# Performance work log

Hardware: AMD Instinct MI355X
Metric: run time of the kernel (lower is better)

## Reference

```python
import jax, jax.numpy as jnp
import numpy as np

N_NODES = 100000
N_EDGES = 1600000
IN_DIM = 256
HIDDEN = 128
N_CLASSES = 40


def gcn_conv(x, W, b, src, dst, n_nodes):
    """torch_geometric GCNConv: transform -> add self-loops -> sym-normalized sum-aggregate -> +bias."""
    h = x @ W  # [N, out]
    loop = jnp.arange(n_nodes, dtype=src.dtype)
    src2 = jnp.concatenate([src, loop])
    dst2 = jnp.concatenate([dst, loop])
    # degree with self-loops (edge weight 1)
    deg = jax.ops.segment_sum(jnp.ones_like(dst2, dtype=h.dtype), dst2, num_segments=n_nodes)
    dinv = jnp.where(deg > 0, jax.lax.rsqrt(deg), 0.0)
    norm = dinv[src2] * dinv[dst2]  # [E+N]
    msg = h[src2] * norm[:, None]   # [E+N, out] gather + scale
    out = jax.ops.segment_sum(msg, dst2, num_segments=n_nodes)
    return out + b


def setup_inputs() -> dict:
    key = jax.random.key(0)
    k1, k2, k3, k4 = jax.random.split(key, 4)
    x = jax.random.normal(k1, (N_NODES, IN_DIM), dtype=jnp.float32)
    edge_index = jax.random.randint(k2, (2, N_EDGES), 0, N_NODES, dtype=jnp.int64)
    W1 = jax.random.normal(k3, (IN_DIM, HIDDEN), dtype=jnp.float32) * (1.0 / np.sqrt(IN_DIM))
    b1 = jnp.zeros((HIDDEN,), dtype=jnp.float32)
    W2 = jax.random.normal(k4, (HIDDEN, N_CLASSES), dtype=jnp.float32) * (1.0 / np.sqrt(HIDDEN))
    b2 = jnp.zeros((N_CLASSES,), dtype=jnp.float32)
    return {"x": x, "edge_index": edge_index, "W1": W1, "b1": b1, "W2": W2, "b2": b2}


def reference(x, edge_index, W1, b1, W2, b2):
    src, dst = edge_index[0], edge_index[1]
    h = gcn_conv(x, W1, b1, src, dst, N_NODES)
    h = jax.nn.relu(h)
    # dropout p=0.5 is identity in eval mode
    out = gcn_conv(h, W2, b2, src, dst, N_NODES)
    return out
```

## Files before the change

### kernel.cpp

```cpp
#include <hip/hip_runtime.h>
#include <hip/hip_bf16.h>
#include <hip/hip_fp16.h>

#define N_NODES 100000
#define N_EDGES 1600000
#define IN_DIM 256
#define HIDDEN 128
#define NCLS 40
#define NCLS_PAD 48

#define N_BUCKETS 256
#define NPB 391
#define BCAP 8192
#define EPT 16
#define BIN_WG 4096
#define BIN_BLOCKS 391

typedef __attribute__((ext_vector_type(8))) _Float16 half8;
typedef __attribute__((ext_vector_type(4))) _Float16 half4f;
typedef __attribute__((ext_vector_type(4))) float floatx4;


__global__ __launch_bounds__(256) void k_bin(const int* __restrict__ src, const int* __restrict__ dst,
                                             int* __restrict__ bfill,
                                             unsigned long long* __restrict__ bpair,
                                             const float* __restrict__ W1, __half* __restrict__ W1T,
                                             const float* __restrict__ W2, __half* __restrict__ W2T) {
    const int t = threadIdx.x;
    if (blockIdx.x >= BIN_BLOCKS) {
        int wb = blockIdx.x - BIN_BLOCKS;
        if (wb < 128) {
            int i = wb * 256 + t;
            int k = i >> 7, n = i & 127;
            W1T[n * IN_DIM + k] = __float2half_rn(W1[i]);
        } else {
            for (int i = t; i < NCLS_PAD * HIDDEN; i += 256) {
                int n = i >> 7, k = i & 127;
                W2T[n * HIDDEN + k] = (n < NCLS) ? __float2half_rn(W2[k * NCLS + n]) : __float2half_rn(0.f);
            }
        }
        return;
    }
    __shared__ int hist[N_BUCKETS];
    __shared__ int bstart[N_BUCKETS];
    __shared__ int gbase[N_BUCKETS];
    __shared__ unsigned long long stage[BIN_WG];
    __shared__ unsigned char bid[BIN_WG];
    hist[t] = 0;
    __syncthreads();
    const long e0 = (long)blockIdx.x * BIN_WG;
    const int n_valid = (int)min((long)BIN_WG, (long)N_EDGES - e0);
    int msrc[EPT], mdst[EPT], moff[EPT];
    #pragma unroll
    for (int i = 0; i < EPT; i++) {
        long e = e0 + t + i * 256;
        if (e < N_EDGES) {
            msrc[i] = src[e];
            mdst[i] = dst[e];
            moff[i] = atomicAdd(&hist[mdst[i] / NPB], 1);
        } else {
            mdst[i] = -1;
        }
    }
    __syncthreads();
    if (t < 64) {
        int carry = 0;
        #pragma unroll
        for (int c = 0; c < 4; c++) {
            int idx = c * 64 + t;
            int hv = hist[idx];
            int s = hv;
            #pragma unroll
            for (int d2 = 1; d2 < 64; d2 <<= 1) {
                int u = __shfl_up(s, d2, 64);
                if (t >= d2) s += u;
            }
            bstart[idx] = carry + (s - hv);
            carry += __shfl(s, 63, 64);
        }
    }
    __syncthreads();
    int h = hist[t];
    gbase[t] = (h > 0) ? atomicAdd(&bfill[t], h) : 0;
    #pragma unroll
    for (int i = 0; i < EPT; i++) {
        if (mdst[i] >= 0) {
            int b = mdst[i] / NPB;
            int pos = bstart[b] + moff[i];
            stage[pos] = ((unsigned long long)(unsigned)mdst[i] << 32) | (unsigned)msrc[i];
            bid[pos] = (unsigned char)b;
        }
    }
    __syncthreads();
    for (int i = t; i < n_valid; i += 256) {
        int b = bid[i];
        int dest = gbase[b] + (i - bstart[b]);
        bpair[(long)b * BCAP + dest] = stage[i];
    }
}


__global__ __launch_bounds__(256) void k_build(const int* __restrict__ bfill,
                                               const unsigned long long* __restrict__ bpair,
                                               int* __restrict__ row_ptr, float* __restrict__ dinv,
                                               int* __restrict__ col) {
    __shared__ int h[NPB];
    __shared__ int pfx[NPB];
    __shared__ int sred[4];
    const int b  = blockIdx.x;
    const int nb = b * NPB;
    const int nn = min(NPB, N_NODES - nb);
    const int t  = threadIdx.x;
    int v = (t < b) ? bfill[t] : 0;
    #pragma unroll
    for (int dl = 32; dl > 0; dl >>= 1) v += __shfl_down(v, dl, 64);
    if ((t & 63) == 0) sred[t >> 6] = v;
    for (int i = t; i < NPB; i += 256) h[i] = 0;
    __syncthreads();
    const int base_b = sred[0] + sred[1] + sred[2] + sred[3];
    const int n = bfill[b];
    for (int i = t; i < n; i += 256) {
        int dd = (int)(bpair[(long)b * BCAP + i] >> 32);
        atomicAdd(&h[dd - nb], 1);
    }
    __syncthreads();
    if (t < 64) {
        int carry = 0;
        #pragma unroll
        for (int c = 0; c < (NPB + 63) / 64; c++) {
            int idx = c * 64 + t;
            int hv = (idx < nn) ? h[idx] : 0;
            int s = hv;
            #pragma unroll
            for (int d2 = 1; d2 < 64; d2 <<= 1) {
                int u = __shfl_up(s, d2, 64);
                if (t >= d2) s += u;
            }
            if (idx < nn) {
                int ex = base_b + carry + (s - hv);
                pfx[idx] = ex;
                row_ptr[nb + idx] = ex;
                dinv[nb + idx] = rsqrtf((float)(hv + 1));
            }
            carry += __shfl(s, 63, 64);
        }
    }
    __syncthreads();
    for (int i = t; i < nn; i += 256) h[i] = 0;
    __syncthreads();
    for (int i = t; i < n; i += 256) {
        unsigned long long p = bpair[(long)b * BCAP + i];
        int dd = (int)(p >> 32);
        int ss = (int)(p & 0xFFFFFFFFu);
        int pos = pfx[dd - nb] + atomicAdd(&h[dd - nb], 1);
        col[pos] = ss;
    }
    if (b == 0 && t == 0) row_ptr[N_NODES] = N_EDGES;
}


__global__ __launch_bounds__(256) void k_gemm1(const float* __restrict__ X,
                                               const __half* __restrict__ W1T,
                                               const float* __restrict__ dinv,
                                               __half* __restrict__ H1s) {
    __shared__ __align__(16) _Float16 Asm[128][72];
    __shared__ __align__(16) _Float16 Bsm[128][72];
    const int tid  = threadIdx.x;
    const int wave = tid >> 6;
    const int lane = tid & 63;
    const int m16  = lane & 15;
    const int kq   = lane >> 4;
    const int row0 = blockIdx.x * 128;

    floatx4 acc[2][8];
    #pragma unroll
    for (int mt = 0; mt < 2; mt++)
        #pragma unroll
        for (int i = 0; i < 8; i++) acc[mt][i] = (floatx4)0.f;

    for (int kc = 0; kc < 4; kc++) {
        #pragma unroll
        for (int it = 0; it < 4; it++) {
            int u = tid + it * 256;
            int r = u >> 3, j = u & 7;
            int gr = row0 + r;
            float4 x0 = make_float4(0.f, 0.f, 0.f, 0.f), x1 = x0;
            if (gr < N_NODES) {
                const float* p = &X[(long)gr * IN_DIM + kc * 64 + j * 8];
                x0 = *(const float4*)p;
                x1 = *(const float4*)(p + 4);
            }
            half8 h;
            h[0] = (_Float16)x0.x; h[1] = (_Float16)x0.y; h[2] = (_Float16)x0.z; h[3] = (_Float16)x0.w;
            h[4] = (_Float16)x1.x; h[5] = (_Float16)x1.y; h[6] = (_Float16)x1.z; h[7] = (_Float16)x1.w;
            *(half8*)&Asm[r][j * 8] = h;
        }
        #pragma unroll
        for (int it = 0; it < 4; it++) {
            int u = tid + it * 256;
            int n = u >> 3, j = u & 7;
            float4 w = *(const float4*)&W1T[n * IN_DIM + kc * 64 + j * 8];
            *(float4*)&Bsm[n][j * 8] = w;
        }
        __syncthreads();
        #pragma unroll
        for (int ks = 0; ks < 2; ks++) {
            half8 a0 = *(const half8*)&Asm[wave * 32 + m16][ks * 32 + kq * 8];
            half8 a1 = *(const half8*)&Asm[wave * 32 + 16 + m16][ks * 32 + kq * 8];
            #pragma unroll
            for (int nt = 0; nt < 8; nt++) {
                half8 b = *(const half8*)&Bsm[nt * 16 + m16][ks * 32 + kq * 8];
                acc[0][nt] = __builtin_amdgcn_mfma_f32_16x16x32_f16(a0, b, acc[0][nt], 0, 0, 0);
                acc[1][nt] = __builtin_amdgcn_mfma_f32_16x16x32_f16(a1, b, acc[1][nt], 0, 0, 0);
            }
        }
        __syncthreads();
    }
    #pragma unroll
    for (int mt = 0; mt < 2; mt++) {
        const int gr0 = row0 + wave * 32 + mt * 16 + kq * 4;
        float dd[4];
        #pragma unroll
        for (int r = 0; r < 4; r++) dd[r] = (gr0 + r < N_NODES) ? dinv[gr0 + r] : 0.f;
        #pragma unroll
        for (int nt = 0; nt < 8; nt++) {
            int c = nt * 16 + m16;
            #pragma unroll
            for (int r = 0; r < 4; r++) {
                if (gr0 + r < N_NODES)
                    H1s[(long)(gr0 + r) * HIDDEN + c] = __float2half_rn(dd[r] * acc[mt][nt][r]);
            }
        }
    }
}


__global__ __launch_bounds__(256) void k_agg1(const __half* __restrict__ H1s,
                                              const int* __restrict__ row_ptr,
                                              const int* __restrict__ col,
                                              const float* __restrict__ dinv,
                                              const float* __restrict__ b1,
                                              __half* __restrict__ H1a) {
    int d = blockIdx.x * 4 + (threadIdx.x >> 6);
    int lane = threadIdx.x & 63;
    int e0 = row_ptr[d], e1 = row_ptr[d + 1];
    const __half2* base = (const __half2*)H1s;
    float ax = 0.f, ay = 0.f;
    int e = e0;
    for (; e + 3 < e1; e += 4) {
        int s0 = col[e], s1 = col[e + 1], s2 = col[e + 2], s3 = col[e + 3];
        float2 f0 = __half22float2(base[(long)s0 * 64 + lane]);
        float2 f1 = __half22float2(base[(long)s1 * 64 + lane]);
        float2 f2 = __half22float2(base[(long)s2 * 64 + lane]);
        float2 f3 = __half22float2(base[(long)s3 * 64 + lane]);
        ax += f0.x + f1.x + f2.x + f3.x;
        ay += f0.y + f1.y + f2.y + f3.y;
    }
    for (; e < e1; e++) {
        float2 f = __half22float2(base[(long)col[e] * 64 + lane]);
        ax += f.x; ay += f.y;
    }
    float2 fs = __half22float2(base[(long)d * 64 + lane]);
    ax += fs.x; ay += fs.y;
    float dd = dinv[d];
    float2 bb = ((const float2*)b1)[lane];
    float ox = fmaxf(dd * ax + bb.x, 0.f);
    float oy = fmaxf(dd * ay + bb.y, 0.f);
    ((__half2*)H1a)[(long)d * 64 + lane] = __halves2half2(__float2half_rn(ox), __float2half_rn(oy));
}


__global__ __launch_bounds__(256) void k_gemm2(const __half* __restrict__ H1a,
                                               const __half* __restrict__ W2T,
                                               const float* __restrict__ dinv,
                                               __half* __restrict__ H2s) {
    const int wave = threadIdx.x >> 6;
    const int lane = threadIdx.x & 63;
    const int m16  = lane & 15;
    const int kq   = lane >> 4;
    const int rowa = min(blockIdx.x * 64 + wave * 16 + m16, N_NODES - 1);

    floatx4 acc[3];
    #pragma unroll
    for (int i = 0; i < 3; i++) acc[i] = (floatx4)0.f;

    #pragma unroll
    for (int ks = 0; ks < 4; ks++) {
        half8 a = *(const half8*)&H1a[(long)rowa * HIDDEN + ks * 32 + kq * 8];
        #pragma unroll
        for (int nt = 0; nt < 3; nt++) {
            half8 b = *(const half8*)&W2T[(nt * 16 + m16) * HIDDEN + ks * 32 + kq * 8];
            acc[nt] = __builtin_amdgcn_mfma_f32_16x16x32_f16(a, b, acc[nt], 0, 0, 0);
        }
    }
    const int gr0 = blockIdx.x * 64 + wave * 16 + kq * 4;
    float dd[4];
    #pragma unroll
    for (int r = 0; r < 4; r++) dd[r] = (gr0 + r < N_NODES) ? dinv[gr0 + r] : 0.f;
    #pragma unroll
    for (int nt = 0; nt < 3; nt++) {
        int c = nt * 16 + m16;
        if (c < NCLS) {
            #pragma unroll
            for (int r = 0; r < 4; r++) {
                if (gr0 + r < N_NODES)
                    H2s[(long)(gr0 + r) * NCLS + c] = __float2half_rn(dd[r] * acc[nt][r]);
            }
        }
    }
}


__global__ __launch_bounds__(256) void k_agg2(const __half* __restrict__ H2s,
                                              const int* __restrict__ row_ptr,
                                              const int* __restrict__ col,
                                              const float* __restrict__ dinv,
                                              const float* __restrict__ b2,
                                              float* __restrict__ out) {
    const int wave = threadIdx.x >> 6;
    const int lane = threadIdx.x & 63;
    const int g = lane / 10;
    const int f = lane - g * 10;
    const int d = blockIdx.x * 24 + wave * 6 + g;
    const bool act = (g < 6) && (d < N_NODES);
    int e0 = 0, e1 = 0;
    if (act) { e0 = row_ptr[d]; e1 = row_ptr[d + 1]; }
    const half4f* base4 = (const half4f*)H2s;
    float s0 = 0.f, s1 = 0.f, s2 = 0.f, s3 = 0.f;
    int e = e0;
    while (__any(e < e1)) {
        if (e < e1) {
            half4f v = base4[(long)col[e] * 10 + f];
            s0 += (float)v[0]; s1 += (float)v[1]; s2 += (float)v[2]; s3 += (float)v[3];
        }
        if (e + 1 < e1) {
            half4f v = base4[(long)col[e + 1] * 10 + f];
            s0 += (float)v[0]; s1 += (float)v[1]; s2 += (float)v[2]; s3 += (float)v[3];
        }
        e += 2;
    }
    if (act) {
        half4f v = base4[(long)d * 10 + f];
        s0 += (float)v[0]; s1 += (float)v[1]; s2 += (float)v[2]; s3 += (float)v[3];
        float dd = dinv[d];
        float4 bb = ((const float4*)b2)[f];
        float4 o = make_float4(dd * s0 + bb.x, dd * s1 + bb.y, dd * s2 + bb.z, dd * s3 + bb.w);
        ((float4*)out)[(long)d * 10 + f] = o;
    }
}


extern "C" void kernel_launch(void* const* d_in, const int* in_sizes, int n_in,
                              void* d_out, int out_size, void* d_ws, size_t ws_size,
                              hipStream_t stream) {
    const float* x  = (const float*)d_in[0];
    const int*   ei = (const int*)d_in[1];
    const float* W1 = (const float*)d_in[2];
    const float* b1 = (const float*)d_in[3];
    const float* W2 = (const float*)d_in[4];
    const float* b2 = (const float*)d_in[5];
    const int* srcE = ei;
    const int* dstE = ei + N_EDGES;

    int*   row_ptr = (int*)d_ws;
    int*   bfill   = row_ptr + 100032;
    int*   col     = bfill + 256;
    float* dinv    = (float*)(col + N_EDGES);
    __half* H1s    = (__half*)(dinv + 100032);
    __half* H1a    = H1s + (long)N_NODES * HIDDEN;
    __half* H2s    = H1a + (long)N_NODES * HIDDEN;
    __half* W1T    = H2s + (long)N_NODES * NCLS;
    __half* W2T    = W1T + IN_DIM * HIDDEN;
    unsigned long long* bpair = (unsigned long long*)H1s;

    hipMemsetAsync(bfill, 0, N_BUCKETS * sizeof(int), stream);

    k_bin   <<<BIN_BLOCKS + 129, 256, 0, stream>>>(srcE, dstE, bfill, bpair, W1, W1T, W2, W2T);
    k_build <<<N_BUCKETS, 256, 0, stream>>>(bfill, bpair, row_ptr, dinv, col);

    k_gemm1 <<<(N_NODES + 127) / 128, 256, 0, stream>>>(x, W1T, dinv, H1s);
    k_agg1  <<<N_NODES / 4, 256, 0, stream>>>(H1s, row_ptr, col, dinv, b1, H1a);
    k_gemm2 <<<(N_NODES + 63) / 64, 256, 0, stream>>>(H1a, W2T, dinv, H2s);
    k_agg2  <<<(N_NODES + 23) / 24, 256, 0, stream>>>(H2s, row_ptr, col, dinv, b2, (float*)d_out);
}
```

Measured before the change: 375.1 us.

## Fuse edge binning with GEMM1 and aggregation1 with GEMM2, defer dinv scaling

Edge binning and the first dense GEMM now run as two block groups of a single launch, so the GEMM no longer waits on degree construction. Because the GEMM no longer has dinv, the per-row dinv scaling of H1 moves into the CSR build kernel as an extra read-modify-write pass. The first aggregation is fused with the second GEMM through a 16-row shared tile, which removes the H1a intermediate buffer and one launch. A prep kernel replaces the memset, and bpair gets its own workspace region instead of aliasing H1s, at the cost of an extra full pass over H1s and a fused kernel with lower MFMA utilisation.

```diff
diff --git a/kernel.cpp b/kernel.cpp
--- a/kernel.cpp
+++ b/kernel.cpp
@@ -15,87 +15,165 @@
 #define EPT 16
 #define BIN_WG 4096
 #define BIN_BLOCKS 391
+#define GEMM1_BLOCKS 782
 
 typedef __attribute__((ext_vector_type(8))) _Float16 half8;
 typedef __attribute__((ext_vector_type(4))) _Float16 half4f;
 typedef __attribute__((ext_vector_type(4))) float floatx4;
 
 
-__global__ __launch_bounds__(256) void k_bin(const int* __restrict__ src, const int* __restrict__ dst,
-                                             int* __restrict__ bfill,
-                                             unsigned long long* __restrict__ bpair,
-                                             const float* __restrict__ W1, __half* __restrict__ W1T,
-                                             const float* __restrict__ W2, __half* __restrict__ W2T) {
+__global__ __launch_bounds__(256) void k_prep(const float* __restrict__ W1, __half* __restrict__ W1T,
+                                              const float* __restrict__ W2, __half* __restrict__ W2T,
+                                              int* __restrict__ bfill) {
     const int t = threadIdx.x;
-    if (blockIdx.x >= BIN_BLOCKS) {
-        int wb = blockIdx.x - BIN_BLOCKS;
-        if (wb < 128) {
-            int i = wb * 256 + t;
-            int k = i >> 7, n = i & 127;
-            W1T[n * IN_DIM + k] = __float2half_rn(W1[i]);
-        } else {
-            for (int i = t; i < NCLS_PAD * HIDDEN; i += 256) {
-                int n = i >> 7, k = i & 127;
-                W2T[n * HIDDEN + k] = (n < NCLS) ? __float2half_rn(W2[k * NCLS + n]) : __float2half_rn(0.f);
-            }
+    if (blockIdx.x < 128) {
+        int i = blockIdx.x * 256 + t;
+        int k = i >> 7, n = i & 127;
+        W1T[n * IN_DIM + k] = __float2half_rn(W1[i]);
+    } else if (blockIdx.x == 128) {
+        for (int i = t; i < NCLS_PAD * HIDDEN; i += 256) {
+            int n = i >> 7, k = i & 127;
+            W2T[n * HIDDEN + k] = (n < NCLS) ? __float2half_rn(W2[k * NCLS + n]) : __float2half_rn(0.f);
+        }
+    } else {
+        bfill[t] = 0;
+    }
+}
+
+
+__global__ __launch_bounds__(256) void k_binmm(const int* __restrict__ src, const int* __restrict__ dst,
+                                               int* __restrict__ bfill,
+                                               unsigned long long* __restrict__ bpair,
+                                               const float* __restrict__ X,
+                                               const __half* __restrict__ W1T,
+                                               __half* __restrict__ H1s) {
+    __shared__ __align__(16) char smraw[39936];
+    const int t = threadIdx.x;
+
+    if (blockIdx.x < BIN_BLOCKS) {
+        int* hist   = (int*)smraw;
+        int* bstart = hist + 256;
+        int* gbase  = bstart + 256;
+        unsigned long long* stage = (unsigned long long*)(smraw + 3072);
+        unsigned char* bid = (unsigned char*)(smraw + 3072 + 32768);
+        hist[t] = 0;
+        __syncthreads();
+        const long e0 = (long)blockIdx.x * BIN_WG;
+        const int n_valid = (int)min((long)BIN_WG, (long)N_EDGES - e0);
+        int msrc[EPT], mdst[EPT], moff[EPT];
+        #pragma unroll
+        for (int i = 0; i < EPT; i++) {
+            long e = e0 + t + i * 256;
+            if (e < N_EDGES) {
+                msrc[i] = src[e];
+                mdst[i] = dst[e];
+                moff[i] = atomicAdd(&hist[mdst[i] / NPB], 1);
+            } else {
+                mdst[i] = -1;
+            }
+        }
+        __syncthreads();
+        if (t < 64) {
+            int carry = 0;
+            #pragma unroll
+            for (int c = 0; c < 4; c++) {
+                int idx = c * 64 + t;
+                int hv = hist[idx];
+                int s = hv;
+                #pragma unroll
+                for (int d2 = 1; d2 < 64; d2 <<= 1) {
+                    int u = __shfl_up(s, d2, 64);
+                    if (t >= d2) s += u;
+                }
+                bstart[idx] = carry + (s - hv);
+                carry += __shfl(s, 63, 64);
+            }
+        }
+        __syncthreads();
+        int h = hist[t];
+        gbase[t] = (h > 0) ? atomicAdd(&bfill[t], h) : 0;
+        #pragma unroll
+        for (int i = 0; i < EPT; i++) {
+            if (mdst[i] >= 0) {
+                int b = mdst[i] / NPB;
+                int pos = bstart[b] + moff[i];
+                stage[pos] = ((unsigned long long)(unsigned)mdst[i] << 32) | (unsigned)msrc[i];
+                bid[pos] = (unsigned char)b;
+            }
+        }
+        __syncthreads();
+        for (int i = t; i < n_valid; i += 256) {
+            int b = bid[i];
+            int dest = gbase[b] + (i - bstart[b]);
+            bpair[(long)b * BCAP + dest] = stage[i];
         }
         return;
     }
-    __shared__ int hist[N_BUCKETS];
-    __shared__ int bstart[N_BUCKETS];
-    __shared__ int gbase[N_BUCKETS];
-    __shared__ unsigned long long stage[BIN_WG];
-    __shared__ unsigned char bid[BIN_WG];
-    hist[t] = 0;
-    __syncthreads();
-    const long e0 = (long)blockIdx.x * BIN_WG;
-    const int n_valid = (int)min((long)BIN_WG, (long)N_EDGES - e0);
-    int msrc[EPT], mdst[EPT], moff[EPT];
+
+    _Float16 (*Asm)[72] = (_Float16(*)[72])smraw;
+    _Float16 (*Bsm)[72] = (_Float16(*)[72])(smraw + 128 * 72 * 2);
+    const int wave = t >> 6;
+    const int lane = t & 63;
+    const int m16  = lane & 15;
+    const int kq   = lane >> 4;
+    const int row0 = (blockIdx.x - BIN_BLOCKS) * 128;
+
+    floatx4 acc[2][8];
     #pragma unroll
-    for (int i = 0; i < EPT; i++) {
-        long e = e0 + t + i * 256;
-        if (e < N_EDGES) {
-            msrc[i] = src[e];
-            mdst[i] = dst[e];
-            moff[i] = atomicAdd(&hist[mdst[i] / NPB], 1);
-        } else {
-            mdst[i] = -1;
-        }
-    }
-    __syncthreads();
-    if (t < 64) {
-        int carry = 0;
-        #pragma unroll
-        for (int c = 0; c < 4; c++) {
-            int idx = c * 64 + t;
-            int hv = hist[idx];
-            int s = hv;
-            #pragma unroll
-            for (int d2 = 1; d2 < 64; d2 <<= 1) {
-                int u = __shfl_up(s, d2, 64);
-                if (t >= d2) s += u;
-            }
-            bstart[idx] = carry + (s - hv);
-            carry += __shfl(s, 63, 64);
-        }
-    }
-    __syncthreads();
-    int h = hist[t];
-    gbase[t] = (h > 0) ? atomicAdd(&bfill[t], h) : 0;
+    for (int mt = 0; mt < 2; mt++)
+        #pragma unroll
+        for (int i = 0; i < 8; i++) acc[mt][i] = (floatx4)0.f;
+
+    for (int kc = 0; kc < 4; kc++) {
+        #pragma unroll
+        for (int it = 0; it < 4; it++) {
+            int u = t + it * 256;
+            int r = u >> 3, j = u & 7;
+            int gr = row0 + r;
+            float4 x0 = make_float4(0.f, 0.f, 0.f, 0.f), x1 = x0;
+            if (gr < N_NODES) {
+                const float* p = &X[(long)gr * IN_DIM + kc * 64 + j * 8];
+                x0 = *(const float4*)p;
+                x1 = *(const float4*)(p + 4);
+            }
+            half8 hh;
+            hh[0] = (_Float16)x0.x; hh[1] = (_Float16)x0.y; hh[2] = (_Float16)x0.z; hh[3] = (_Float16)x0.w;
+            hh[4] = (_Float16)x1.x; hh[5] = (_Float16)x1.y; hh[6] = (_Float16)x1.z; hh[7] = (_Float16)x1.w;
+            *(half8*)&Asm[r][j * 8] = hh;
+        }
+        #pragma unroll
+        for (int it = 0; it < 4; it++) {
+            int u = t + it * 256;
+            int n = u >> 3, j = u & 7;
+            float4 w = *(const float4*)&W1T[n * IN_DIM + kc * 64 + j * 8];
+            *(float4*)&Bsm[n][j * 8] = w;
+        }
+        __syncthreads();
+        #pragma unroll
+        for (int ks = 0; ks < 2; ks++) {
+            half8 a0 = *(const half8*)&Asm[wave * 32 + m16][ks * 32 + kq * 8];
+            half8 a1 = *(const half8*)&Asm[wave * 32 + 16 + m16][ks * 32 + kq * 8];
+            #pragma unroll
+            for (int nt = 0; nt < 8; nt++) {
+                half8 b = *(const half8*)&Bsm[nt * 16 + m16][ks * 32 + kq * 8];
+                acc[0][nt] = __builtin_amdgcn_mfma_f32_16x16x32_f16(a0, b, acc[0][nt], 0, 0, 0);
+                acc[1][nt] = __builtin_amdgcn_mfma_f32_16x16x32_f16(a1, b, acc[1][nt], 0, 0, 0);
+            }
+        }
+        __syncthreads();
+    }
     #pragma unroll
-    for (int i = 0; i < EPT; i++) {
-        if (mdst[i] >= 0) {
-            int b = mdst[i] / NPB;
-            int pos = bstart[b] + moff[i];
-            stage[pos] = ((unsigned long long)(unsigned)mdst[i] << 32) | (unsigned)msrc[i];
-            bid[pos] = (unsigned char)b;
-        }
-    }
-    __syncthreads();
-    for (int i = t; i < n_valid; i += 256) {
-        int b = bid[i];
-        int dest = gbase[b] + (i - bstart[b]);
-        bpair[(long)b * BCAP + dest] = stage[i];
+    for (int mt = 0; mt < 2; mt++) {
+        const int gr0 = row0 + wave * 32 + mt * 16 + kq * 4;
+        #pragma unroll
+        for (int nt = 0; nt < 8; nt++) {
+            int c = nt * 16 + m16;
+            #pragma unroll
+            for (int r = 0; r < 4; r++) {
+                if (gr0 + r < N_NODES)
+                    H1s[(long)(gr0 + r) * HIDDEN + c] = __float2half_rn(acc[mt][nt][r]);
+            }
+        }
     }
 }
 
@@ -103,9 +181,10 @@
 __global__ __launch_bounds__(256) void k_build(const int* __restrict__ bfill,
                                                const unsigned long long* __restrict__ bpair,
                                                int* __restrict__ row_ptr, float* __restrict__ dinv,
-                                               int* __restrict__ col) {
+                                               int* __restrict__ col, __half* __restrict__ H1s) {
     __shared__ int h[NPB];
     __shared__ int pfx[NPB];
+    __shared__ float sdinv[NPB];
     __shared__ int sred[4];
     const int b  = blockIdx.x;
     const int nb = b * NPB;
@@ -140,7 +219,9 @@
                 int ex = base_b + carry + (s - hv);
                 pfx[idx] = ex;
                 row_ptr[nb + idx] = ex;
-                dinv[nb + idx] = rsqrtf((float)(hv + 1));
+                float dv = rsqrtf((float)(hv + 1));
+                dinv[nb + idx] = dv;
+                sdinv[idx] = dv;
             }
             carry += __shfl(s, 63, 64);
         }
@@ -155,157 +236,76 @@
         int pos = pfx[dd - nb] + atomicAdd(&h[dd - nb], 1);
         col[pos] = ss;
     }
+    __half2* Hp = (__half2*)H1s;
+    for (int i = t; i < nn * 64; i += 256) {
+        int r = i >> 6, o = i & 63;
+        float dv = sdinv[r];
+        float2 f = __half22float2(Hp[(long)(nb + r) * 64 + o]);
+        Hp[(long)(nb + r) * 64 + o] = __halves2half2(__float2half_rn(f.x * dv), __float2half_rn(f.y * dv));
+    }
     if (b == 0 && t == 0) row_ptr[N_NODES] = N_EDGES;
 }
 
 
-__global__ __launch_bounds__(256) void k_gemm1(const float* __restrict__ X,
-                                               const __half* __restrict__ W1T,
-                                               const float* __restrict__ dinv,
-                                               __half* __restrict__ H1s) {
-    __shared__ __align__(16) _Float16 Asm[128][72];
-    __shared__ __align__(16) _Float16 Bsm[128][72];
-    const int tid  = threadIdx.x;
-    const int wave = tid >> 6;
-    const int lane = tid & 63;
-    const int m16  = lane & 15;
-    const int kq   = lane >> 4;
-    const int row0 = blockIdx.x * 128;
-
-    floatx4 acc[2][8];
-    #pragma unroll
-    for (int mt = 0; mt < 2; mt++)
-        #pragma unroll
-        for (int i = 0; i < 8; i++) acc[mt][i] = (floatx4)0.f;
-
-    for (int kc = 0; kc < 4; kc++) {
-        #pragma unroll
-        for (int it = 0; it < 4; it++) {
-            int u = tid + it * 256;
-            int r = u >> 3, j = u & 7;
-            int gr = row0 + r;
-            float4 x0 = make_float4(0.f, 0.f, 0.f, 0.f), x1 = x0;
-            if (gr < N_NODES) {
-                const float* p = &X[(long)gr * IN_DIM + kc * 64 + j * 8];
-                x0 = *(const float4*)p;
-                x1 = *(const float4*)(p + 4);
-            }
-            half8 h;
-            h[0] = (_Float16)x0.x; h[1] = (_Float16)x0.y; h[2] = (_Float16)x0.z; h[3] = (_Float16)x0.w;
-            h[4] = (_Float16)x1.x; h[5] = (_Float16)x1.y; h[6] = (_Float16)x1.z; h[7] = (_Float16)x1.w;
-            *(half8*)&Asm[r][j * 8] = h;
-        }
-        #pragma unroll
-        for (int it = 0; it < 4; it++) {
-            int u = tid + it * 256;
-            int n = u >> 3, j = u & 7;
-            float4 w = *(const float4*)&W1T[n * IN_DIM + kc * 64 + j * 8];
-            *(float4*)&Bsm[n][j * 8] = w;
-        }
-        __syncthreads();
-        #pragma unroll
-        for (int ks = 0; ks < 2; ks++) {
-            half8 a0 = *(const half8*)&Asm[wave * 32 + m16][ks * 32 + kq * 8];
-            half8 a1 = *(const half8*)&Asm[wave * 32 + 16 + m16][ks * 32 + kq * 8];
-            #pragma unroll
-            for (int nt = 0; nt < 8; nt++) {
-                half8 b = *(const half8*)&Bsm[nt * 16 + m16][ks * 32 + kq * 8];
-                acc[0][nt] = __builtin_amdgcn_mfma_f32_16x16x32_f16(a0, b, acc[0][nt], 0, 0, 0);
-                acc[1][nt] = __builtin_amdgcn_mfma_f32_16x16x32_f16(a1, b, acc[1][nt], 0, 0, 0);
-            }
-        }
-        __syncthreads();
-    }
-    #pragma unroll
-    for (int mt = 0; mt < 2; mt++) {
-        const int gr0 = row0 + wave * 32 + mt * 16 + kq * 4;
-        float dd[4];
-        #pragma unroll
-        for (int r = 0; r < 4; r++) dd[r] = (gr0 + r < N_NODES) ? dinv[gr0 + r] : 0.f;
-        #pragma unroll
-        for (int nt = 0; nt < 8; nt++) {
-            int c = nt * 16 + m16;
-            #pragma unroll
-            for (int r = 0; r < 4; r++) {
-                if (gr0 + r < N_NODES)
-                    H1s[(long)(gr0 + r) * HIDDEN + c] = __float2half_rn(dd[r] * acc[mt][nt][r]);
-            }
-        }
-    }
-}
-
-
-__global__ __launch_bounds__(256) void k_agg1(const __half* __restrict__ H1s,
-                                              const int* __restrict__ row_ptr,
-                                              const int* __restrict__ col,
-                                              const float* __restrict__ dinv,
-                                              const float* __restrict__ b1,
-                                              __half* __restrict__ H1a) {
-    int d = blockIdx.x * 4 + (threadIdx.x >> 6);
-    int lane = threadIdx.x & 63;
-    int e0 = row_ptr[d], e1 = row_ptr[d + 1];
-    const __half2* base = (const __half2*)H1s;
-    float ax = 0.f, ay = 0.f;
-    int e = e0;
-    for (; e + 3 < e1; e += 4) {
-        int s0 = col[e], s1 = col[e + 1], s2 = col[e + 2], s3 = col[e + 3];
-        float2 f0 = __half22float2(base[(long)s0 * 64 + lane]);
-        float2 f1 = __half22float2(base[(long)s1 * 64 + lane]);
-        float2 f2 = __half22float2(base[(long)s2 * 64 + lane]);
-        float2 f3 = __half22float2(base[(long)s3 * 64 + lane]);
-        ax += f0.x + f1.x + f2.x + f3.x;
-        ay += f0.y + f1.y + f2.y + f3.y;
-    }
-    for (; e < e1; e++) {
-        float2 f = __half22float2(base[(long)col[e] * 64 + lane]);
-        ax += f.x; ay += f.y;
-    }
-    float2 fs = __half22float2(base[(long)d * 64 + lane]);
-    ax += fs.x; ay += fs.y;
-    float dd = dinv[d];
-    float2 bb = ((const float2*)b1)[lane];
-    float ox = fmaxf(dd * ax + bb.x, 0.f);
-    float oy = fmaxf(dd * ay + bb.y, 0.f);
-    ((__half2*)H1a)[(long)d * 64 + lane] = __halves2half2(__float2half_rn(ox), __float2half_rn(oy));
-}
-
-
-__global__ __launch_bounds__(256) void k_gemm2(const __half* __restrict__ H1a,
-                                               const __half* __restrict__ W2T,
-                                               const float* __restrict__ dinv,
-                                               __half* __restrict__ H2s) {
+__global__ __launch_bounds__(256) void k_agg1g2(const __half* __restrict__ H1s,
+                                                const int* __restrict__ row_ptr,
+                                                const int* __restrict__ col,
+                                                const float* __restrict__ dinv,
+                                                const float* __restrict__ b1,
+                                                const __half* __restrict__ W2T,
+                                                __half* __restrict__ H2s) {
+    __shared__ __align__(16) _Float16 rows[16][136];
     const int wave = threadIdx.x >> 6;
     const int lane = threadIdx.x & 63;
-    const int m16  = lane & 15;
-    const int kq   = lane >> 4;
-    const int rowa = min(blockIdx.x * 64 + wave * 16 + m16, N_NODES - 1);
-
-    floatx4 acc[3];
+    const __half2* base = (const __half2*)H1s;
+    const float2 bb = ((const float2*)b1)[lane];
+    const int d00 = blockIdx.x * 16 + wave * 4;
+
     #pragma unroll
-    for (int i = 0; i < 3; i++) acc[i] = (floatx4)0.f;
-
-    #pragma unroll
-    for (int ks = 0; ks < 4; ks++) {
-        half8 a = *(const half8*)&H1a[(long)rowa * HIDDEN + ks * 32 + kq * 8];
-        #pragma unroll
-        for (int nt = 0; nt < 3; nt++) {
-            half8 b = *(const half8*)&W2T[(nt * 16 + m16) * HIDDEN + ks * 32 + kq * 8];
-            acc[nt] = __builtin_amdgcn_mfma_f32_16x16x32_f16(a, b, acc[nt], 0, 0, 0);
-        }
-    }
-    const int gr0 = blockIdx.x * 64 + wave * 16 + kq * 4;
-    float dd[4];
-    #pragma unroll
-    for (int r = 0; r < 4; r++) dd[r] = (gr0 + r < N_NODES) ? dinv[gr0 + r] : 0.f;
-    #pragma unroll
-    for (int nt = 0; nt < 3; nt++) {
-        int c = nt * 16 + m16;
+    for (int i = 0; i < 4; i++) {
+        const int d = d00 + i;
+        int e0 = row_ptr[d], e1 = row_ptr[d + 1];
+        float ax = 0.f, ay = 0.f;
+        int e = e0;
+        for (; e + 3 < e1; e += 4) {
+            int s0 = col[e], s1 = col[e + 1], s2 = col[e + 2], s3 = col[e + 3];
+            float2 f0 = __half22float2(base[(long)s0 * 64 + lane]);
+            float2 f1 = __half22float2(base[(long)s1 * 64 + lane]);
+            float2 f2 = __half22float2(base[(long)s2 * 64 + lane]);
+            float2 f3 = __half22float2(base[(long)s3 * 64 + lane]);
+            ax += f0.x + f1.x + f2.x + f3.x;
+            ay += f0.y + f1.y + f2.y + f3.y;
+        }
+        for (; e < e1; e++) {
+            float2 f = __half22float2(base[(long)col[e] * 64 + lane]);
+            ax += f.x; ay += f.y;
+        }
+        float2 fs = __half22float2(base[(long)d * 64 + lane]);
+        ax += fs.x; ay += fs.y;
+        const float dd = dinv[d];
+        float ox = fmaxf(dd * ax + bb.x, 0.f) * dd;
+        float oy = fmaxf(dd * ay + bb.y, 0.f) * dd;
+        *(__half2*)&rows[wave * 4 + i][lane * 2] =
+            __halves2half2(__float2half_rn(ox), __float2half_rn(oy));
+    }
+    __syncthreads();
+
+    if (wave < 3) {
+        const int m16 = lane & 15;
+        const int kq  = lane >> 4;
+        floatx4 acc = (floatx4)0.f;
+        #pragma unroll
+        for (int ks = 0; ks < 4; ks++) {
+            half8 a = *(const half8*)&rows[m16][ks * 32 + kq * 8];
+            half8 b = *(const half8*)&W2T[(wave * 16 + m16) * HIDDEN + ks * 32 + kq * 8];
+            acc = __builtin_amdgcn_mfma_f32_16x16x32_f16(a, b, acc, 0, 0, 0);
+        }
+        const int c = wave * 16 + m16;
         if (c < NCLS) {
-            #pragma unroll
-            for (int r = 0; r < 4; r++) {
-                if (gr0 + r < N_NODES)
-                    H2s[(long)(gr0 + r) * NCLS + c] = __float2half_rn(dd[r] * acc[nt][r]);
-            }
+            const int gr0 = blockIdx.x * 16 + kq * 4;
+            #pragma unroll
+            for (int r = 0; r < 4; r++)
+                H2s[(long)(gr0 + r) * NCLS + c] = __float2half_rn(acc[r]);
         }
     }
 }
@@ -343,8 +343,8 @@
         half4f v = base4[(long)d * 10 + f];
         s0 += (float)v[0]; s1 += (float)v[1]; s2 += (float)v[2]; s3 += (float)v[3];
         float dd = dinv[d];
-        float4 bb = ((const float4*)b2)[f];
-        float4 o = make_float4(dd * s0 + bb.x, dd * s1 + bb.y, dd * s2 + bb.z, dd * s3 + bb.w);
+        float4 bbv = ((const float4*)b2)[f];
+        float4 o = make_float4(dd * s0 + bbv.x, dd * s1 + bbv.y, dd * s2 + bbv.z, dd * s3 + bbv.w);
         ((float4*)out)[(long)d * 10 + f] = o;
     }
 }
@@ -367,19 +367,14 @@
     int*   col     = bfill + 256;
     float* dinv    = (float*)(col + N_EDGES);
     __half* H1s    = (__half*)(dinv + 100032);
-    __half* H1a    = H1s + (long)N_NODES * HIDDEN;
-    __half* H2s    = H1a + (long)N_NODES * HIDDEN;
+    __half* H2s    = H1s + (long)N_NODES * HIDDEN;
     __half* W1T    = H2s + (long)N_NODES * NCLS;
     __half* W2T    = W1T + IN_DIM * HIDDEN;
-    unsigned long long* bpair = (unsigned long long*)H1s;
-
-    hipMemsetAsync(bfill, 0, N_BUCKETS * sizeof(int), stream);
-
-    k_bin   <<<BIN_BLOCKS + 129, 256, 0, stream>>>(srcE, dstE, bfill, bpair, W1, W1T, W2, W2T);
-    k_build <<<N_BUCKETS, 256, 0, stream>>>(bfill, bpair, row_ptr, dinv, col);
-
-    k_gemm1 <<<(N_NODES + 127) / 128, 256, 0, stream>>>(x, W1T, dinv, H1s);
-    k_agg1  <<<N_NODES / 4, 256, 0, stream>>>(H1s, row_ptr, col, dinv, b1, H1a);
-    k_gemm2 <<<(N_NODES + 63) / 64, 256, 0, stream>>>(H1a, W2T, dinv, H2s);
-    k_agg2  <<<(N_NODES + 23) / 24, 256, 0, stream>>>(H2s, row_ptr, col, dinv, b2, (float*)d_out);
-}
+    unsigned long long* bpair = (unsigned long long*)(W2T + NCLS_PAD * HIDDEN);
+
+    k_prep   <<<130, 256, 0, stream>>>(W1, W1T, W2, W2T, bfill);
+    k_binmm  <<<BIN_BLOCKS + GEMM1_BLOCKS, 256, 0, stream>>>(srcE, dstE, bfill, bpair, x, W1T, H1s);
+    k_build  <<<N_BUCKETS, 256, 0, stream>>>(bfill, bpair, row_ptr, dinv, col, H1s);
+    k_agg1g2 <<<N_NODES / 16, 256, 0, stream>>>(H1s, row_ptr, col, dinv, b1, W2T, H2s);
+    k_agg2   <<<(N_NODES + 23) / 24, 256, 0, stream>>>(H2s, row_ptr, col, dinv, b2, (float*)d_out);
+}
```

Result: faster. 358.8 us (-4.4%).
